# Performance work log

Measured on AMD Instinct MI355X. Metric: run time of the kernel, lower is better.

## Reference

```python
import jax, jax.numpy as jnp
import numpy as np

B, L, D_IN, D_MODEL, D_STATE, D_DISCR, KER = 2, 1024, 512, 1024, 16, 64, 4


def setup_inputs() -> dict:
    ks = jax.random.split(jax.random.key(0), 9)
    s = 0.02
    return {
        "seq": jax.random.normal(ks[0], (B, L, D_IN), jnp.float32),
        "W_in": jax.random.normal(ks[1], (2 * D_MODEL, D_IN), jnp.float32) * s,
        "W_out": jax.random.normal(ks[2], (D_IN, D_MODEL), jnp.float32) * s,
        "W_B": jax.random.normal(ks[3], (D_STATE, D_MODEL), jnp.float32) * s,
        "W_C": jax.random.normal(ks[4], (D_STATE, D_MODEL), jnp.float32) * s,
        "W_D1": jax.random.normal(ks[5], (D_DISCR, D_MODEL), jnp.float32) * s,
        "W_D2": jax.random.normal(ks[6], (D_MODEL, D_DISCR), jnp.float32) * s,
        "conv_w": jax.random.normal(ks[7], (D_MODEL, 1, KER), jnp.float32) * 0.1,
        "conv_b": jax.random.normal(ks[8], (D_MODEL,), jnp.float32) * 0.01,
        "A": jnp.tile(jnp.arange(1, D_STATE + 1, dtype=jnp.float32), (D_MODEL, 1)),
        "D": jnp.ones((D_MODEL,), jnp.float32),
    }


def _causal_depthwise_conv(x, w, b):
    # x: [B, L, D] -> torch Conv1d(groups=D, padding=KER-1) truncated to first L outputs
    x = jnp.swapaxes(x, 1, 2)  # [B, D, L]
    y = jax.lax.conv_general_dilated(
        x, w, window_strides=(1,), padding=[(KER - 1, 0)],
        dimension_numbers=("NCH", "OIH", "NCH"), feature_group_count=D_MODEL)
    y = y + b[None, :, None]
    return jnp.swapaxes(y, 1, 2)  # [B, L, D]


def _ssm(x, W_B, W_C, W_D1, W_D2, A, D):
    # x: [B, L, D]
    exp_negA = jnp.exp(-A)                                  # [D, S]
    Bm = jnp.einsum("bld,sd->bls", x, W_B)                  # [B, L, S]
    Cm = jnp.einsum("bld,sd->bls", x, W_C)                  # [B, L, S]
    delta = jax.nn.softplus(D + jnp.einsum("ble,de->bld", jnp.einsum("bld,ed->ble", x, W_D1), W_D2))  # [B, L, D]
    A_bar = exp_negA[None, None] * delta[..., None]         # [B, L, D, S]
    X = Bm[:, :, None, :] * delta[..., None] * x[..., None]  # [B, L, D, S]

    def comb(c1, c2):
        a1, x1 = c1
        a2, x2 = c2
        return a1 * a2, a2 * x1 + x2

    _, h = jax.lax.associative_scan(comb, (A_bar, X), axis=1)  # h: [B, L, D, S]
    y = jnp.einsum("blds,bls->bld", h, Cm)
    return y + D * x


def reference(seq, W_in, W_out, W_B, W_C, W_D1, W_D2, conv_w, conv_b, A, D):
    ab = jnp.einsum("bli,oi->blo", seq, W_in)   # [B, L, 2*D_MODEL]
    a, b = ab[..., :D_MODEL], ab[..., D_MODEL:]
    a = jax.nn.silu(_causal_depthwise_conv(a, conv_w, conv_b))
    a = _ssm(a, W_B, W_C, W_D1, W_D2, A, D)
    out = a * jax.nn.silu(b)
    return jnp.einsum("bld,od->blo", out, W_out)  # [B, L, D_IN]
```

## Files before the change

### kernel.cpp

```cpp
#include <hip/hip_runtime.h>
#include <hip/hip_bf16.h>

typedef short short8 __attribute__((ext_vector_type(8)));
typedef short short4v __attribute__((ext_vector_type(4)));
typedef float float4v __attribute__((ext_vector_type(4)));

#define B_   2
#define L_   1024
#define DIN  512
#define DM   1024
#define DS   16
#define DD   64
#define KER_ 4
#define NROW (B_*L_)

#define SD   4
#define SC   64
#define SLC  16
#define SDP  5

__device__ __forceinline__ float silu_f(float v){ return v / (1.f + expf(-v)); }

__device__ __forceinline__ short2 f2bf2(float a, float b) {
  __hip_bfloat162 h = __float22bfloat162_rn(float2{a, b});
  union { __hip_bfloat162 h; short2 s; } u; u.h = h; return u.s;
}
__device__ __forceinline__ short f2bf1(float a) {
  __hip_bfloat16 h = __float2bfloat16(a);
  union { __hip_bfloat16 h; short s; } u; u.h = h; return u.s;
}
__device__ __forceinline__ short8 pack8(const float4& x0, const float4& x1) {
  short2 s0 = f2bf2(x0.x, x0.y), s1 = f2bf2(x0.z, x0.w);
  short2 s2 = f2bf2(x1.x, x1.y), s3 = f2bf2(x1.z, x1.w);
  return short8{ s0.x, s0.y, s1.x, s1.y, s2.x, s2.y, s3.x, s3.y };
}
__device__ __forceinline__ float bf2f(short s) {
  union { unsigned u; float f; } v; v.u = ((unsigned)(unsigned short)s) << 16; return v.f;
}

__global__ __launch_bounds__(256)
void gemm1_k(const float* __restrict__ seq, const float* __restrict__ Win,
             __hip_bfloat16* __restrict__ ab, float* __restrict__ pall) {
  __shared__ short As[64 * 40];
  __shared__ short Bs[64 * 40];
  const int tid  = threadIdx.x;
  {
    int zi = (blockIdx.y * 32 + blockIdx.x) * 256 + tid;
    if (zi < NROW * 96) pall[zi] = 0.f;
  }
  const int lane = tid & 63;
  const int wave = tid >> 6;
  const int r16  = lane & 15;
  const int quad = lane >> 4;
  const int m0 = blockIdx.y * 64;
  const int n0 = blockIdx.x * 64;
  const int wm = wave & 1, wn = wave >> 1;
  float4v acc[2][2];
#pragma unroll
  for (int i = 0; i < 2; i++)
#pragma unroll
    for (int j = 0; j < 2; j++) acc[i][j] = (float4v){0.f, 0.f, 0.f, 0.f};
  float4 pf0[2], pf1[2];
  auto ldu = [&](int j, int k0) {
    int u = tid + j * 256;
    const float4* p;
    if (u < 256) { int row = u >> 2, q = u & 3;
      p = (const float4*)(seq + (size_t)(m0 + row) * DIN + k0 + q * 8);
    } else { int v = u - 256; int row = v >> 2, q = v & 3;
      p = (const float4*)(Win + (size_t)(n0 + row) * DIN + k0 + q * 8);
    }
    pf0[j] = p[0]; pf1[j] = p[1];
  };
  auto stu = [&](int j) {
    int u = tid + j * 256;
    short8 s = pack8(pf0[j], pf1[j]);
    if (u < 256) { int row = u >> 2, q = u & 3; *(short8*)&As[row * 40 + q * 8] = s; }
    else { int v = u - 256; int row = v >> 2, q = v & 3; *(short8*)&Bs[row * 40 + q * 8] = s; }
  };
  ldu(0, 0); ldu(1, 0);
  for (int k0 = 0; k0 < DIN; k0 += 32) {
    stu(0); stu(1);
    __syncthreads();
    if (k0 + 32 < DIN) { ldu(0, k0 + 32); ldu(1, k0 + 32); }
    short8 afr[2], bfr[2];
#pragma unroll
    for (int mi = 0; mi < 2; mi++)
      afr[mi] = *(const short8*)&As[(wm * 32 + mi * 16 + r16) * 40 + quad * 8];
#pragma unroll
    for (int ni = 0; ni < 2; ni++)
      bfr[ni] = *(const short8*)&Bs[(wn * 32 + ni * 16 + r16) * 40 + quad * 8];
#pragma unroll
    for (int mi = 0; mi < 2; mi++)
#pragma unroll
      for (int ni = 0; ni < 2; ni++)
        acc[mi][ni] = __builtin_amdgcn_mfma_f32_16x16x32_bf16(afr[mi], bfr[ni], acc[mi][ni], 0, 0, 0);
    __syncthreads();
  }
#pragma unroll
  for (int mi = 0; mi < 2; mi++)
#pragma unroll
    for (int ni = 0; ni < 2; ni++) {
      int gn = n0 + wn * 32 + ni * 16 + r16;
#pragma unroll
      for (int r = 0; r < 4; r++) {
        int gm = m0 + wm * 32 + mi * 16 + quad * 4 + r;
        ab[(size_t)gm * (2 * DM) + gn] = __float2bfloat16(acc[mi][ni][r]);
      }
    }
}

__global__ __launch_bounds__(256)
void convproj_k(const __hip_bfloat16* __restrict__ ab, const float* __restrict__ cw,
                const float* __restrict__ cb, const float* __restrict__ WB,
                const float* __restrict__ WC, const float* __restrict__ WD1,
                float* __restrict__ xt, short* __restrict__ gt,
                float* __restrict__ pall) {
  __shared__ char smraw[12800];
  const int blk = blockIdx.x;
  const int tid = threadIdx.x;

  if (blk < 1024) {
    short* tile = (short*)smraw;
    const int n0 = (blk & 31) * 64;
    const int d0 = (blk >> 5) * 64;
    const int l0 = n0 & (L_ - 1);
    for (int u = tid; u < 67 * 8; u += 256) {
      int r = u >> 3, c8 = u & 7;
      int l = l0 - 3 + r;
      short8 v = short8{0, 0, 0, 0, 0, 0, 0, 0};
      if (l >= 0 && r < 67)
        v = *(const short8*)(ab + (size_t)(n0 - l0 + l) * (2 * DM) + d0 + c8 * 8);
      *(short8*)&tile[r * 74 + c8 * 8] = v;
    }
    __syncthreads();
    const int i  = tid & 63;
    const int dl = tid >> 6;
    if (d0 < DM) {
#pragma unroll 4
      for (int p = 0; p < 16; p++) {
        int dc = p * 4 + dl;
        int d  = d0 + dc;
        float4 w = *(const float4*)(cw + d * 4);
        float a = cb[d];
        a += bf2f(tile[(i + 0) * 74 + dc]) * w.x;
        a += bf2f(tile[(i + 1) * 74 + dc]) * w.y;
        a += bf2f(tile[(i + 2) * 74 + dc]) * w.z;
        a += bf2f(tile[(i + 3) * 74 + dc]) * w.w;
        xt[(size_t)d * NROW + n0 + i] = silu_f(a);
      }
    } else {
#pragma unroll 4
      for (int p = 0; p < 16; p++) {
        int dc = p * 4 + dl;
        gt[(size_t)(d0 - DM + dc) * NROW + n0 + i] = tile[(i + 3) * 74 + dc];
      }
    }
    return;
  }

  short* As = (short*)smraw;
  short* Bs = As + 64 * 40;
  const int b2   = blk - 1024;
  const int lane = tid & 63;
  const int wave = tid >> 6;
  const int r16  = lane & 15;
  const int quad = lane >> 4;
  const int m0   = (b2 & 31) * 64;
  const int kbeg = (b2 >> 5) * 128;
  float4v acc[6];
#pragma unroll
  for (int i = 0; i < 6; i++) acc[i] = (float4v){0.f, 0.f, 0.f, 0.f};

  short8 ta[KER_];
  float4 pf0[2], pf1[2];
  const int arow = tid >> 2, aq = tid & 3;
  const int an = m0 + arow, al = an & (L_ - 1), abq = an >> 10;

  auto ldu_a = [&](int k0) {
#pragma unroll
    for (int t = 0; t < KER_; t++) {
      int ll = al - (KER_ - 1) + t;
      if (ll >= 0)
        ta[t] = *(const short8*)(ab + (size_t)(abq * L_ + ll) * (2 * DM) + k0 + aq * 8);
      else
        ta[t] = short8{0, 0, 0, 0, 0, 0, 0, 0};
    }
  };
  auto stu_a = [&](int k0) {
    float r8[8];
#pragma unroll
    for (int e = 0; e < 8; e++) {
      int d = k0 + aq * 8 + e;
      float4 w = *(const float4*)(cw + d * 4);
      float a = cb[d];
      a += bf2f(ta[0][e]) * w.x;
      a += bf2f(ta[1][e]) * w.y;
      a += bf2f(ta[2][e]) * w.z;
      a += bf2f(ta[3][e]) * w.w;
      r8[e] = silu_f(a);
    }
    *(short8*)&As[arow * 40 + aq * 8] =
        pack8(float4{r8[0], r8[1], r8[2], r8[3]}, float4{r8[4], r8[5], r8[6], r8[7]});
  };
  auto ldu_b = [&](int j, int k0) {
    int u = tid + j * 256;
    if (u >= 640) return;
    int v = u - 256, row = v >> 2, q = v & 3;
    const float* bp = (row < 16) ? (WB + (size_t)row * DM)
                    : (row < 32) ? (WC + (size_t)(row - 16) * DM)
                                 : (WD1 + (size_t)(row - 32) * DM);
    const float4* p = (const float4*)(bp + k0 + q * 8);
    pf0[j - 1] = p[0]; pf1[j - 1] = p[1];
  };
  auto stu_b = [&](int j) {
    int u = tid + j * 256;
    if (u >= 640) return;
    int v = u - 256, row = v >> 2, q = v & 3;
    *(short8*)&Bs[row * 40 + q * 8] = pack8(pf0[j - 1], pf1[j - 1]);
  };

  ldu_a(kbeg); ldu_b(1, kbeg); ldu_b(2, kbeg);
  for (int k0 = kbeg; k0 < kbeg + 128; k0 += 32) {
    stu_a(k0); stu_b(1); stu_b(2);
    __syncthreads();
    if (k0 + 32 < kbeg + 128) { ldu_a(k0 + 32); ldu_b(1, k0 + 32); ldu_b(2, k0 + 32); }
    short8 afr = *(const short8*)&As[(wave * 16 + r16) * 40 + quad * 8];
#pragma unroll
    for (int ni = 0; ni < 6; ni++) {
      short8 bfr = *(const short8*)&Bs[(ni * 16 + r16) * 40 + quad * 8];
      acc[ni] = __builtin_amdgcn_mfma_f32_16x16x32_bf16(afr, bfr, acc[ni], 0, 0, 0);
    }
    __syncthreads();
  }
#pragma unroll
  for (int ni = 0; ni < 6; ni++) {
    int gn = ni * 16 + r16;
#pragma unroll
    for (int r = 0; r < 4; r++) {
      int gm = m0 + wave * 16 + quad * 4 + r;
      atomicAdd(&pall[(size_t)gm * 96 + gn], acc[ni][r]);
    }
  }
}

__global__ __launch_bounds__(256)
void delta_k(const float* __restrict__ t1, const float* __restrict__ WD2,
             const float* __restrict__ Dv, float* __restrict__ dltT) {
  __shared__ short As[64 * 40];
  __shared__ short Bs[64 * 40];
  const int tid  = threadIdx.x;
  const int lane = tid & 63;
  const int wave = tid >> 6;
  const int r16  = lane & 15;
  const int quad = lane >> 4;
  const int m0 = blockIdx.y * 64;
  const int n0 = blockIdx.x * 64;
  const int wm = wave & 1, wn = wave >> 1;
  float4v acc[2][2];
#pragma unroll
  for (int i = 0; i < 2; i++)
#pragma unroll
    for (int j = 0; j < 2; j++) acc[i][j] = (float4v){0.f, 0.f, 0.f, 0.f};
  float4 pf0[2], pf1[2];
  auto ldu = [&](int j, int k0) {
    int u = tid + j * 256;
    const float4* p;
    if (u < 256) { int row = u >> 2, q = u & 3;
      p = (const float4*)(t1 + (size_t)(m0 + row) * 96 + k0 + q * 8);
    } else { int v = u - 256; int row = v >> 2, q = v & 3;
      p = (const float4*)(WD2 + (size_t)(n0 + row) * DD + k0 + q * 8);
    }
    pf0[j] = p[0]; pf1[j] = p[1];
  };
  auto stu = [&](int j) {
    int u = tid + j * 256;
    short8 s = pack8(pf0[j], pf1[j]);
    if (u < 256) { int row = u >> 2, q = u & 3; *(short8*)&As[row * 40 + q * 8] = s; }
    else { int v = u - 256; int row = v >> 2, q = v & 3; *(short8*)&Bs[row * 40 + q * 8] = s; }
  };
  ldu(0, 0); ldu(1, 0);
  for (int k0 = 0; k0 < DD; k0 += 32) {
    stu(0); stu(1);
    __syncthreads();
    if (k0 + 32 < DD) { ldu(0, k0 + 32); ldu(1, k0 + 32); }
    short8 afr[2], bfr[2];
#pragma unroll
    for (int mi = 0; mi < 2; mi++)
      afr[mi] = *(const short8*)&As[(wm * 32 + mi * 16 + r16) * 40 + quad * 8];
#pragma unroll
    for (int ni = 0; ni < 2; ni++)
      bfr[ni] = *(const short8*)&Bs[(wn * 32 + ni * 16 + r16) * 40 + quad * 8];
#pragma unroll
    for (int mi = 0; mi < 2; mi++)
#pragma unroll
      for (int ni = 0; ni < 2; ni++)
        acc[mi][ni] = __builtin_amdgcn_mfma_f32_16x16x32_bf16(afr[mi], bfr[ni], acc[mi][ni], 0, 0, 0);
    __syncthreads();
  }
#pragma unroll
  for (int mi = 0; mi < 2; mi++)
#pragma unroll
    for (int ni = 0; ni < 2; ni++) {
      int gn = n0 + wn * 32 + ni * 16 + r16;
      float dvn = Dv[gn];
#pragma unroll
      for (int r = 0; r < 4; r++) {
        int gm = m0 + wm * 32 + mi * 16 + quad * 4 + r;
        float v = acc[mi][ni][r] + dvn;
        v = fmaxf(v, 0.f) + log1pf(expf(-fabsf(v)));
        dltT[(size_t)gn * NROW + gm] = v;
      }
    }
}

__global__ __launch_bounds__(256)
void scan_fused_k(const float* __restrict__ xt, const float* __restrict__ dltT,
                  const float* __restrict__ pall, const float* __restrict__ A,
                  const float* __restrict__ Dv, const short* __restrict__ gt,
                  short* __restrict__ soutb) {
  __shared__ float Pl[SC][DS][SDP];
  __shared__ float Hl[SC][DS][SDP];
  const int blk = blockIdx.x;
  const int b   = blk >> 8;
  const int d0  = (blk & 255) * SD;
  const int dd  = threadIdx.x & (SD - 1);
  const int c   = threadIdx.x >> 2;
  const int d   = d0 + dd;

  float e[DS];
#pragma unroll
  for (int s = 0; s < DS; s++) e[s] = expf(-A[d * DS + s]);
  const int nbase = b * L_ + c * SLC;
  const float* xrow = xt   + (size_t)d * NROW;
  const float* drow = dltT + (size_t)d * NROW;
  const short* grow = gt   + (size_t)d * NROW;

  float h[DS], p[DS];
#pragma unroll
  for (int s = 0; s < DS; s++) { h[s] = 0.f; p[s] = 1.f; }
#pragma unroll
  for (int q = 0; q < SLC / 4; q++) {
    const int n = nbase + q * 4;
    float4 x4 = *(const float4*)(xrow + n);
    float4 d4 = *(const float4*)(drow + n);
    float4 bq[4][4];
#pragma unroll
    for (int t = 0; t < 4; t++) {
      const float4* pp = (const float4*)(pall + (size_t)(n + t) * 96);
      bq[t][0] = pp[0]; bq[t][1] = pp[1]; bq[t][2] = pp[2]; bq[t][3] = pp[3];
    }
#pragma unroll
    for (int t = 0; t < 4; t++) {
      float dl = (&d4.x)[t], xv = (&x4.x)[t];
      float dx = dl * xv;
      float bmv[DS] = { bq[t][0].x, bq[t][0].y, bq[t][0].z, bq[t][0].w,
                        bq[t][1].x, bq[t][1].y, bq[t][1].z, bq[t][1].w,
                        bq[t][2].x, bq[t][2].y, bq[t][2].z, bq[t][2].w,
                        bq[t][3].x, bq[t][3].y, bq[t][3].z, bq[t][3].w };
#pragma unroll
      for (int s = 0; s < DS; s++) {
        float a_ = e[s] * dl;
        h[s] = a_ * h[s] + bmv[s] * dx;
        p[s] *= a_;
      }
    }
  }
#pragma unroll
  for (int s = 0; s < DS; s++) { Pl[c][s][dd] = p[s]; Hl[c][s][dd] = h[s]; }
  __syncthreads();

  if (threadIdx.x < DS * SD) {
    int s2  = threadIdx.x >> 2;
    int dd2 = threadIdx.x & (SD - 1);
    float H = 0.f;
    for (int c2 = 0; c2 < SC; c2++) {
      float pp = Pl[c2][s2][dd2];
      float hh = Hl[c2][s2][dd2];
      Pl[c2][s2][dd2] = H;
      H = pp * H + hh;
    }
  }
  __syncthreads();

#pragma unroll
  for (int s = 0; s < DS; s++) h[s] = Pl[c][s][dd];
  float Dd = Dv[d];
#pragma unroll
  for (int q = 0; q < SLC / 4; q++) {
    const int n = nbase + q * 4;
    float4 x4 = *(const float4*)(xrow + n);
    float4 d4 = *(const float4*)(drow + n);
    short4v g4 = *(const short4v*)(grow + n);
    float4 bq[4][4], cq[4][4];
#pragma unroll
    for (int t = 0; t < 4; t++) {
      const float4* pp = (const float4*)(pall + (size_t)(n + t) * 96);
      bq[t][0] = pp[0]; bq[t][1] = pp[1]; bq[t][2] = pp[2]; bq[t][3] = pp[3];
      cq[t][0] = pp[4]; cq[t][1] = pp[5]; cq[t][2] = pp[6]; cq[t][3] = pp[7];
    }
#pragma unroll
    for (int t = 0; t < 4; t++) {
      float dl = (&d4.x)[t], xv = (&x4.x)[t];
      float dx = dl * xv;
      float bmv[DS] = { bq[t][0].x, bq[t][0].y, bq[t][0].z, bq[t][0].w,
                        bq[t][1].x, bq[t][1].y, bq[t][1].z, bq[t][1].w,
                        bq[t][2].x, bq[t][2].y, bq[t][2].z, bq[t][2].w,
                        bq[t][3].x, bq[t][3].y, bq[t][3].z, bq[t][3].w };
      float cmv[DS] = { cq[t][0].x, cq[t][0].y, cq[t][0].z, cq[t][0].w,
                        cq[t][1].x, cq[t][1].y, cq[t][1].z, cq[t][1].w,
                        cq[t][2].x, cq[t][2].y, cq[t][2].z, cq[t][2].w,
                        cq[t][3].x, cq[t][3].y, cq[t][3].z, cq[t][3].w };
      float y = 0.f;
#pragma unroll
      for (int s = 0; s < DS; s++) {
        h[s] = e[s] * dl * h[s] + bmv[s] * dx;
        y += h[s] * cmv[s];
      }
      y += Dd * xv;
      float g = bf2f(g4[t]);
      soutb[(size_t)(n + t) * DM + d] = f2bf1(y * silu_f(g));
    }
  }
}

__global__ __launch_bounds__(256)
void gemm2_k(const short* __restrict__ soutb, const float* __restrict__ Wout,
             float* __restrict__ out) {
  __shared__ short As[64 * 40];
  __shared__ short Bs[32 * 40];
  const int tid  = threadIdx.x;
  const int lane = tid & 63;
  const int wave = tid >> 6;
  const int r16  = lane & 15;
  const int quad = lane >> 4;
  const int m0 = blockIdx.y * 64;
  const int n0 = blockIdx.x * 32;
  const int wm = wave & 1, wn = wave >> 1;
  float4v acc[2];
  acc[0] = (float4v){0.f, 0.f, 0.f, 0.f};
  acc[1] = (float4v){0.f, 0.f, 0.f, 0.f};
  short8 pa;
  float4 pf0, pf1;
  auto ldu = [&](int k0) {
    {
      int row = tid >> 2, q = tid & 3;
      pa = *(const short8*)(soutb + (size_t)(m0 + row) * DM + k0 + q * 8);
    }
    if (tid < 128) {
      int row = tid >> 2, q = tid & 3;
      const float4* p = (const float4*)(Wout + (size_t)(n0 + row) * DM + k0 + q * 8);
      pf0 = p[0]; pf1 = p[1];
    }
  };
  auto stu = [&]() {
    { int row = tid >> 2, q = tid & 3; *(short8*)&As[row * 40 + q * 8] = pa; }
    if (tid < 128) { int row = tid >> 2, q = tid & 3; *(short8*)&Bs[row * 40 + q * 8] = pack8(pf0, pf1); }
  };
  ldu(0);
  for (int k0 = 0; k0 < DM; k0 += 32) {
    stu();
    __syncthreads();
    if (k0 + 32 < DM) ldu(k0 + 32);
    short8 afr[2], bfr;
    afr[0] = *(const short8*)&As[(wm * 32 + r16) * 40 + quad * 8];
    afr[1] = *(const short8*)&As[(wm * 32 + 16 + r16) * 40 + quad * 8];
    bfr    = *(const short8*)&Bs[(wn * 16 + r16) * 40 + quad * 8];
    acc[0] = __builtin_amdgcn_mfma_f32_16x16x32_bf16(afr[0], bfr, acc[0], 0, 0, 0);
    acc[1] = __builtin_amdgcn_mfma_f32_16x16x32_bf16(afr[1], bfr, acc[1], 0, 0, 0);
    __syncthreads();
  }
#pragma unroll
  for (int mi = 0; mi < 2; mi++)
#pragma unroll
    for (int r = 0; r < 4; r++)
      out[(size_t)(m0 + wm * 32 + mi * 16 + quad * 4 + r) * DIN + n0 + wn * 16 + r16] = acc[mi][r];
}

extern "C" void kernel_launch(void* const* d_in, const int* in_sizes, int n_in,
                              void* d_out, int out_size, void* d_ws, size_t ws_size,
                              hipStream_t stream) {
  const float* seq  = (const float*)d_in[0];
  const float* Win  = (const float*)d_in[1];
  const float* Wout = (const float*)d_in[2];
  const float* WB   = (const float*)d_in[3];
  const float* WC   = (const float*)d_in[4];
  const float* WD1  = (const float*)d_in[5];
  const float* WD2  = (const float*)d_in[6];
  const float* cw   = (const float*)d_in[7];
  const float* cb   = (const float*)d_in[8];
  const float* A    = (const float*)d_in[9];
  const float* Dv   = (const float*)d_in[10];
  float* out = (float*)d_out;

  float* ws = (float*)d_ws;
  __hip_bfloat16* ab = (__hip_bfloat16*)ws;
  float* xt   = ws   + 2097152;
  short* gt   = (short*)(xt + 2097152);
  float* dltT = (float*)(gt + 2097152);
  float* pall = dltT + 2097152;
  short* soutb = (short*)(pall + 196608);
  float* t1   = pall + 32;

  gemm1_k<<<dim3(32, 32), 256, 0, stream>>>(seq, Win, ab, pall);
  convproj_k<<<1280, 256, 0, stream>>>(ab, cw, cb, WB, WC, WD1, xt, gt, pall);
  delta_k<<<dim3(16, 32), 256, 0, stream>>>(t1, WD2, Dv, dltT);
  scan_fused_k<<<B_ * (DM / SD), 256, 0, stream>>>(xt, dltT, pall, A, Dv, gt, soutb);
  gemm2_k<<<dim3(16, 32), 256, 0, stream>>>(soutb, Wout, out);
}
```

Before: 159.8 us.

## Split scan into more shorter chunks and factor the chunk decay product

```diff
diff --git a/kernel.cpp b/kernel.cpp
--- a/kernel.cpp
+++ b/kernel.cpp
@@ -15,9 +15,8 @@
 #define NROW (B_*L_)
 
 #define SD   4
-#define SC   64
-#define SLC  16
-#define SDP  5
+#define SC   128
+#define SLC  8
 
 __device__ __forceinline__ float silu_f(float v){ return v / (1.f + expf(-v)); }
 
@@ -313,13 +312,13 @@
     }
 }
 
-__global__ __launch_bounds__(256)
+__global__ __launch_bounds__(512, 4)
 void scan_fused_k(const float* __restrict__ xt, const float* __restrict__ dltT,
                   const float* __restrict__ pall, const float* __restrict__ A,
                   const float* __restrict__ Dv, const short* __restrict__ gt,
                   short* __restrict__ soutb) {
-  __shared__ float Pl[SC][DS][SDP];
-  __shared__ float Hl[SC][DS][SDP];
+  __shared__ float Pl[DS * SD][SC + 1];
+  __shared__ float Hl[DS * SD][SC + 1];
   const int blk = blockIdx.x;
   const int b   = blk >> 8;
   const int d0  = (blk & 255) * SD;
@@ -327,17 +326,22 @@
   const int c   = threadIdx.x >> 2;
   const int d   = d0 + dd;
 
-  float e[DS];
-#pragma unroll
-  for (int s = 0; s < DS; s++) e[s] = expf(-A[d * DS + s]);
+  float e[DS], esl[DS];
+#pragma unroll
+  for (int s = 0; s < DS; s++) {
+    float a = A[d * DS + s];
+    e[s]   = expf(-a);
+    esl[s] = expf(-(float)SLC * a);
+  }
   const int nbase = b * L_ + c * SLC;
   const float* xrow = xt   + (size_t)d * NROW;
   const float* drow = dltT + (size_t)d * NROW;
   const short* grow = gt   + (size_t)d * NROW;
 
-  float h[DS], p[DS];
-#pragma unroll
-  for (int s = 0; s < DS; s++) { h[s] = 0.f; p[s] = 1.f; }
+  float h[DS];
+#pragma unroll
+  for (int s = 0; s < DS; s++) h[s] = 0.f;
+  float pdl = 1.f;
 #pragma unroll
   for (int q = 0; q < SLC / 4; q++) {
     const int n = nbase + q * 4;
@@ -353,37 +357,38 @@
     for (int t = 0; t < 4; t++) {
       float dl = (&d4.x)[t], xv = (&x4.x)[t];
       float dx = dl * xv;
+      pdl *= dl;
       float bmv[DS] = { bq[t][0].x, bq[t][0].y, bq[t][0].z, bq[t][0].w,
                         bq[t][1].x, bq[t][1].y, bq[t][1].z, bq[t][1].w,
                         bq[t][2].x, bq[t][2].y, bq[t][2].z, bq[t][2].w,
                         bq[t][3].x, bq[t][3].y, bq[t][3].z, bq[t][3].w };
 #pragma unroll
-      for (int s = 0; s < DS; s++) {
-        float a_ = e[s] * dl;
-        h[s] = a_ * h[s] + bmv[s] * dx;
-        p[s] *= a_;
-      }
-    }
-  }
-#pragma unroll
-  for (int s = 0; s < DS; s++) { Pl[c][s][dd] = p[s]; Hl[c][s][dd] = h[s]; }
+      for (int s = 0; s < DS; s++)
+        h[s] = (e[s] * dl) * h[s] + bmv[s] * dx;
+    }
+  }
+#pragma unroll
+  for (int s = 0; s < DS; s++) {
+    Pl[s * SD + dd][c] = esl[s] * pdl;
+    Hl[s * SD + dd][c] = h[s];
+  }
   __syncthreads();
 
   if (threadIdx.x < DS * SD) {
-    int s2  = threadIdx.x >> 2;
-    int dd2 = threadIdx.x & (SD - 1);
+    float* Prow = &Pl[threadIdx.x][0];
+    float* Hrow = &Hl[threadIdx.x][0];
     float H = 0.f;
     for (int c2 = 0; c2 < SC; c2++) {
-      float pp = Pl[c2][s2][dd2];
-      float hh = Hl[c2][s2][dd2];
-      Pl[c2][s2][dd2] = H;
+      float pp = Prow[c2];
+      float hh = Hrow[c2];
+      Prow[c2] = H;
       H = pp * H + hh;
     }
   }
   __syncthreads();
 
 #pragma unroll
-  for (int s = 0; s < DS; s++) h[s] = Pl[c][s][dd];
+  for (int s = 0; s < DS; s++) h[s] = Pl[s * SD + dd][c];
   float Dd = Dv[d];
 #pragma unroll
   for (int q = 0; q < SLC / 4; q++) {
@@ -413,7 +418,7 @@
       float y = 0.f;
 #pragma unroll
       for (int s = 0; s < DS; s++) {
-        h[s] = e[s] * dl * h[s] + bmv[s] * dx;
+        h[s] = (e[s] * dl) * h[s] + bmv[s] * dx;
         y += h[s] * cmv[s];
       }
       y += Dd * xv;
@@ -504,6 +509,6 @@
   gemm1_k<<<dim3(32, 32), 256, 0, stream>>>(seq, Win, ab, pall);
   convproj_k<<<1280, 256, 0, stream>>>(ab, cw, cb, WB, WC, WD1, xt, gt, pall);
   delta_k<<<dim3(16, 32), 256, 0, stream>>>(t1, WD2, Dv, dltT);
-  scan_fused_k<<<B_ * (DM / SD), 256, 0, stream>>>(xt, dltT, pall, A, Dv, gt, soutb);
+  scan_fused_k<<<B_ * (DM / SD), 512, 0, stream>>>(xt, dltT, pall, A, Dv, gt, soutb);
   gemm2_k<<<dim3(16, 32), 256, 0, stream>>>(soutb, Wout, out);
 }
```

Measured after the change: 162.5 us. No clear change (+1.7%).
